# Kernel tuning notes

Hardware: AMD Instinct MI355X
Metric: run time of the kernel (lower is better)

## Reference

```python
import jax, jax.numpy as jnp
import numpy as np

S, B, H = 2048, 16, 512      # seq_len, batch, hidden_size
L = 4096                     # total labels across batch
SMAX = 16                    # max span length
LAB = 256                    # label_size
V = 32000                    # len(voc)


def setup_inputs() -> dict:
    key = jax.random.key(0)
    ks = jax.random.split(key, 10)
    hidden = jax.random.normal(ks[0], (S, B, H), jnp.float32)
    begins = jax.random.randint(ks[1], (L,), 1, S - SMAX - 1)          # >=1 so begin-1 valid
    lens = jax.random.randint(ks[2], (L,), 1, SMAX + 1)                # span length in [1, SMAX]
    ends = begins + lens                                               # < S so hidden[end] valid
    bids = jax.random.randint(ks[3], (L,), 0, B)
    tags = jax.random.randint(ks[4], (L,), 0, V)
    sc = 0.02
    W1 = jax.random.normal(ks[5], (3 * H, LAB), jnp.float32) * sc
    b1 = jnp.zeros((LAB,), jnp.float32)
    W2 = jax.random.normal(ks[6], (LAB, LAB), jnp.float32) * sc
    b2 = jnp.zeros((LAB,), jnp.float32)
    Wo = jax.random.normal(ks[7], (LAB, V), jnp.float32) * sc
    bo = jnp.zeros((V,), jnp.float32)
    return dict(hidden=hidden, begins=begins, ends=ends, bids=bids, tags=tags,
                W1=W1, b1=b1, W2=W2, b2=b2, Wo=Wo, bo=bo)


def reference(hidden, begins, ends, bids, tags, W1, b1, W2, b2, Wo, bo):
    # --- batched span embed: gather + masked mean + boundary concat ---
    pos = begins[:, None] + jnp.arange(SMAX)            # [L, SMAX]
    valid = (pos < ends[:, None]).astype(hidden.dtype)  # [L, SMAX]
    posc = jnp.minimum(pos, S - 1)
    g = hidden[posc, bids[:, None]]                     # [L, SMAX, H] gather
    span_len = (ends - begins).astype(hidden.dtype)[:, None]
    mean = (g * valid[..., None]).sum(axis=1) / span_len           # [L, H]
    left = hidden[begins - 1, bids]                                 # [L, H]
    right = hidden[ends, bids]                                      # [L, H]
    span_emb = jnp.concatenate([left, mean, right], axis=-1)        # [L, 3H]
    # --- hidden2feature: Linear -> sigmoid -> Linear (dropout = eval identity) ---
    feat = jax.nn.sigmoid(span_emb @ W1 + b1) @ W2 + b2             # [L, LAB]
    # --- SoftmaxLoss: -log_softmax(h2o(feat)).gather(tags).mean() per label ---
    logp = jax.nn.log_softmax(feat @ Wo + bo, axis=-1)              # [L, V]
    per_label = -logp[jnp.arange(L), tags]                          # one tag per label
    return per_label.sum() / (L + 1e-5)
```

## Files before the change

### kernel.cpp

```cpp
#include <hip/hip_runtime.h>
#include <math.h>

#define S 2048
#define B 16
#define H 512
#define L 4096
#define SMAX 16
#define LAB 256
#define V 32000
#define NCH 250
#define LOG2E 1.44269504f

typedef __attribute__((ext_vector_type(8))) short short8;
typedef __attribute__((ext_vector_type(4))) float float4v;

__device__ inline ushort f2bf(float x) {
  union { float f; unsigned u; } c; c.f = x;
  unsigned r = c.u + 0x7fffu + ((c.u >> 16) & 1u);
  return (ushort)(r >> 16);
}
__device__ inline float bf2f(ushort h) {
  union { unsigned u; float f; } c; c.u = ((unsigned)h) << 16;
  return c.f;
}

__global__ __launch_bounds__(256) void prep_kernel(
    const float* __restrict__ hidden, const int* __restrict__ begins,
    const int* __restrict__ ends, const int* __restrict__ bids,
    ushort* __restrict__ spanb, const float* __restrict__ W1,
    ushort* __restrict__ W1b, const float* __restrict__ W2,
    ushort* __restrict__ W2b, const float* __restrict__ Wo,
    ushort* __restrict__ Wob) {
  __shared__ ushort tile[64 * 72];
  int bid = blockIdx.x;
  int t = threadIdx.x;

  if (bid < 2048) {
    int sub = t >> 7, tt = t & 127;
    int l = bid * 2 + sub;
    int b = bids[l], s0 = begins[l], s1 = ends[l];
    const float4* hidv = (const float4*)hidden;
    float4 lf = hidv[((size_t)(s0 - 1) * B + b) * 128 + tt];
    float4 rf = hidv[((size_t)s1 * B + b) * 128 + tt];
    float4 m = make_float4(0.f, 0.f, 0.f, 0.f);
    int len = s1 - s0;
    for (int j = 0; j < len; ++j) {
      float4 g = hidv[((size_t)(s0 + j) * B + b) * 128 + tt];
      m.x += g.x; m.y += g.y; m.z += g.z; m.w += g.w;
    }
    float inv = 1.0f / (float)len;
    ushort* sp = spanb + (size_t)l * 1536;
    ushort4 u;
    u.x = f2bf(lf.x); u.y = f2bf(lf.y); u.z = f2bf(lf.z); u.w = f2bf(lf.w);
    *(ushort4*)&sp[tt * 4] = u;
    u.x = f2bf(m.x * inv); u.y = f2bf(m.y * inv);
    u.z = f2bf(m.z * inv); u.w = f2bf(m.w * inv);
    *(ushort4*)&sp[512 + tt * 4] = u;
    u.x = f2bf(rf.x); u.y = f2bf(rf.y); u.z = f2bf(rf.z); u.w = f2bf(rf.w);
    *(ushort4*)&sp[1024 + tt * 4] = u;
    return;
  }

  const float* src; ushort* dst; int K, N, n0, k0; bool wo = false;
  if (bid < 2144) {
    int u = bid - 2048; src = W1; dst = W1b; K = 1536; N = 256;
    n0 = (u & 3) * 64; k0 = (u >> 2) * 64;
  } else if (bid < 2160) {
    int u = bid - 2144; src = W2; dst = W2b; K = 256; N = 256;
    n0 = (u & 3) * 64; k0 = (u >> 2) * 64;
  } else {
    int u = bid - 2160; src = Wo; dst = Wob; K = 256; N = V;
    n0 = (u % 500) * 64; k0 = (u / 500) * 64; wo = true;
  }
  #pragma unroll
  for (int p = 0; p < 16; ++p) {
    int k = p * 4 + (t >> 6);
    int n = t & 63;
    tile[n * 72 + k] = f2bf(src[(size_t)(k0 + k) * N + n0 + n]);
  }
  __syncthreads();
  if (!wo) {
    #pragma unroll
    for (int p = 0; p < 2; ++p) {
      int idx = p * 256 + t;
      int n = idx >> 3, c = idx & 7;
      *(uint4*)&dst[(size_t)(n0 + n) * K + k0 + c * 8] =
          *(const uint4*)&tile[n * 72 + c * 8];
    }
  } else {
    #pragma unroll
    for (int p = 0; p < 2; ++p) {
      int idx = p * 256 + t;
      int n = idx >> 3, c8 = idx & 7;
      int v = n0 + n, k = k0 + c8 * 8;
      int c = v >> 7, nt = (v >> 4) & 7, lr = v & 15;
      int kh = k >> 7, k4 = (k >> 5) & 3, lq = (k >> 3) & 3;
      size_t f = ((((size_t)c * 2 + kh) * 4 + k4) * 8 + nt) * 64 + lq * 16 + lr;
      *(uint4*)&dst[f * 8] = *(const uint4*)&tile[n * 72 + c8 * 8];
    }
  }
}

__global__ __launch_bounds__(256) void feat_mfma_kernel(
    const ushort* __restrict__ spanb, const ushort* __restrict__ W1b,
    const float* __restrict__ b1, const ushort* __restrict__ W2b,
    const float* __restrict__ b2, ushort* __restrict__ featb,
    float* __restrict__ out) {
  __shared__ ushort Hs[16 * 264];
  int tid = threadIdx.x;
  if (blockIdx.x == 0 && tid == 0) *out = 0.f;
  int w = tid >> 6, lane = tid & 63;
  int lr = lane & 15, lq = lane >> 4;
  int l0 = blockIdx.x * 16;

  const short8* arow = (const short8*)(spanb + (size_t)(l0 + lr) * 1536 + lq * 8);
  const short8* brow[4];
  #pragma unroll
  for (int nt = 0; nt < 4; ++nt)
    brow[nt] = (const short8*)(W1b + (size_t)(w * 64 + nt * 16 + lr) * 1536 + lq * 8);

  float4v acc[4];
  float4v zero = {0.f, 0.f, 0.f, 0.f};
  #pragma unroll
  for (int nt = 0; nt < 4; ++nt) acc[nt] = zero;

  short8 af[2], bf[2][4];
  af[0] = arow[0];
  #pragma unroll
  for (int nt = 0; nt < 4; ++nt) bf[0][nt] = brow[nt][0];

  #pragma unroll
  for (int s = 0; s < 48; ++s) {
    int cur = s & 1, nxt = cur ^ 1;
    if (s < 47) {
      af[nxt] = arow[(s + 1) * 4];
      #pragma unroll
      for (int nt = 0; nt < 4; ++nt) bf[nxt][nt] = brow[nt][(s + 1) * 4];
    }
    #pragma unroll
    for (int nt = 0; nt < 4; ++nt)
      acc[nt] = __builtin_amdgcn_mfma_f32_16x16x32_bf16(
          af[cur], bf[cur][nt], acc[nt], 0, 0, 0);
  }

  {
    #pragma unroll
    for (int nt = 0; nt < 4; ++nt) {
      float b1v = b1[w * 64 + nt * 16 + lr];
      #pragma unroll
      for (int r = 0; r < 4; ++r) {
        int row = lq * 4 + r;
        float h = 1.0f / (1.0f + __expf(-(acc[nt][r] + b1v)));
        Hs[row * 264 + w * 64 + nt * 16 + lr] = f2bf(h);
      }
    }
  }
  __syncthreads();

  const short8* wrow[4];
  #pragma unroll
  for (int nt = 0; nt < 4; ++nt)
    wrow[nt] = (const short8*)(W2b + (size_t)(w * 64 + nt * 16 + lr) * 256 + lq * 8);

  float4v acc2[4];
  #pragma unroll
  for (int nt = 0; nt < 4; ++nt) acc2[nt] = zero;

  short8 bf2[2][4];
  #pragma unroll
  for (int nt = 0; nt < 4; ++nt) bf2[0][nt] = wrow[nt][0];

  #pragma unroll
  for (int s = 0; s < 8; ++s) {
    int cur = s & 1, nxt = cur ^ 1;
    if (s < 7) {
      #pragma unroll
      for (int nt = 0; nt < 4; ++nt) bf2[nxt][nt] = wrow[nt][(s + 1) * 4];
    }
    short8 af2 = *(const short8*)&Hs[lr * 264 + s * 32 + lq * 8];
    #pragma unroll
    for (int nt = 0; nt < 4; ++nt)
      acc2[nt] = __builtin_amdgcn_mfma_f32_16x16x32_bf16(
          af2, bf2[cur][nt], acc2[nt], 0, 0, 0);
  }

  {
    #pragma unroll
    for (int nt = 0; nt < 4; ++nt) {
      float b2v = b2[w * 64 + nt * 16 + lr];
      #pragma unroll
      for (int r = 0; r < 4; ++r) {
        int row = lq * 4 + r;
        int col = w * 64 + nt * 16 + lr;
        featb[(size_t)(l0 + row) * 256 + col] = f2bf(acc2[nt][r] + b2v);
      }
    }
  }
}

__global__ __launch_bounds__(512, 4) void logits2_kernel(
    const ushort* __restrict__ featb, const ushort* __restrict__ Wob,
    const float* __restrict__ bo, float* __restrict__ pz) {
  __shared__ ushort Blds[2][16384];
  int tid = threadIdx.x;
  int w = tid >> 6, lane = tid & 63;
  int lr = lane & 15, lq = lane >> 4;
  int l0 = blockIdx.x * 256;
  int v0 = blockIdx.y * 128;

  const short8* aptr[2];
  #pragma unroll
  for (int mt = 0; mt < 2; ++mt)
    aptr[mt] = (const short8*)(featb +
        (size_t)(l0 + w * 32 + mt * 16 + lr) * 256 + lq * 8);

  float4v acc[2][8];
  float4v zero = {0.f, 0.f, 0.f, 0.f};
  #pragma unroll
  for (int mt = 0; mt < 2; ++mt)
    #pragma unroll
    for (int nt = 0; nt < 8; ++nt) acc[mt][nt] = zero;

  short8 af[2][2];
  #pragma unroll
  for (int mt = 0; mt < 2; ++mt) af[0][mt] = aptr[mt][0];

#define STAGE_HALF(buf, kh)                                                   \
  {                                                                           \
    const uint4* src4 = (const uint4*)(Wob +                                  \
        (size_t)blockIdx.y * 32768 + (size_t)(kh) * 16384);                   \
    _Pragma("unroll")                                                         \
    for (int p = 0; p < 4; ++p) {                                             \
      int idx = p * 512 + tid;                                                \
      __builtin_amdgcn_global_load_lds(                                       \
          (const __attribute__((address_space(1))) unsigned int*)(src4 + idx),\
          (__attribute__((address_space(3))) unsigned int*)                   \
              &Blds[buf][(size_t)idx * 8],                                    \
          16, 0, 0);                                                          \
    }                                                                         \
  }

#define KG_BLOCK(buf, kh)                                                     \
  _Pragma("unroll")                                                           \
  for (int k4 = 0; k4 < 4; ++k4) {                                            \
    int kg = (kh) * 4 + k4;                                                   \
    int cur = kg & 1, nxt = cur ^ 1;                                          \
    if (kg < 7) {                                                             \
      _Pragma("unroll")                                                       \
      for (int mt = 0; mt < 2; ++mt)                                          \
        af[nxt][mt] = aptr[mt][(kg + 1) * 4];                                 \
    }                                                                         \
    short8 bf[8];                                                             \
    _Pragma("unroll")                                                         \
    for (int nt = 0; nt < 8; ++nt)                                            \
      bf[nt] = *(const short8*)                                               \
          &Blds[buf][(size_t)(((k4 * 8 + nt) * 64) + lane) * 8];              \
    __builtin_amdgcn_s_setprio(1);                                            \
    _Pragma("unroll")                                                         \
    for (int mt = 0; mt < 2; ++mt)                                            \
      _Pragma("unroll")                                                       \
      for (int nt = 0; nt < 8; ++nt)                                          \
        acc[mt][nt] = __builtin_amdgcn_mfma_f32_16x16x32_bf16(                \
            af[cur][mt], bf[nt], acc[mt][nt], 0, 0, 0);                       \
    __builtin_amdgcn_s_setprio(0);                                            \
  }

  STAGE_HALF(0, 0);
  __syncthreads();
  STAGE_HALF(1, 1);
  KG_BLOCK(0, 0);
  __syncthreads();
  KG_BLOCK(1, 1);

#undef STAGE_HALF
#undef KG_BLOCK

  float bov[8];
  #pragma unroll
  for (int nt = 0; nt < 8; ++nt)
    bov[nt] = bo[v0 + nt * 16 + lr] * LOG2E;
  float z[2][4];
  #pragma unroll
  for (int mt = 0; mt < 2; ++mt)
    #pragma unroll
    for (int r = 0; r < 4; ++r) z[mt][r] = 0.f;
  #pragma unroll
  for (int mt = 0; mt < 2; ++mt)
    #pragma unroll
    for (int nt = 0; nt < 8; ++nt)
      #pragma unroll
      for (int r = 0; r < 4; ++r)
        z[mt][r] += exp2f(fmaf(acc[mt][nt][r], LOG2E, bov[nt]));
  #pragma unroll
  for (int mt = 0; mt < 2; ++mt)
    #pragma unroll
    for (int r = 0; r < 4; ++r) {
      #pragma unroll
      for (int off = 1; off < 16; off <<= 1)
        z[mt][r] += __shfl_xor(z[mt][r], off);
    }
  if (lr == 0) {
    int ch = blockIdx.y;
    #pragma unroll
    for (int mt = 0; mt < 2; ++mt) {
      float4 v4;
      v4.x = z[mt][0]; v4.y = z[mt][1]; v4.z = z[mt][2]; v4.w = z[mt][3];
      *(float4*)&pz[(size_t)ch * L + l0 + w * 32 + mt * 16 + lq * 4] = v4;
    }
  }
}

__global__ __launch_bounds__(256) void tag_kernel(
    const ushort* __restrict__ featb, const ushort* __restrict__ Wob,
    const float* __restrict__ bo, const int* __restrict__ tags,
    float* __restrict__ tagl) {
  int l = blockIdx.x * 4 + (threadIdx.x >> 6);
  int lane = threadIdx.x & 63;
  int tg = tags[l];
  int c = tg >> 7, nt = (tg >> 4) & 7, lr = tg & 15;
  int k0 = lane << 2;
  int kh = k0 >> 7, k4 = (k0 >> 5) & 3, lq = (k0 >> 3) & 3, e = k0 & 7;
  size_t f = ((((size_t)c * 2 + kh) * 4 + k4) * 8 + nt) * 64 + lq * 16 + lr;
  ushort4 wa = *(const ushort4*)&Wob[f * 8 + e];
  ushort4 fa = *(const ushort4*)&featb[(size_t)l * 256 + k0];
  float s = bf2f(fa.x) * bf2f(wa.x) + bf2f(fa.y) * bf2f(wa.y) +
            bf2f(fa.z) * bf2f(wa.z) + bf2f(fa.w) * bf2f(wa.w);
  #pragma unroll
  for (int off = 1; off < 64; off <<= 1) s += __shfl_xor(s, off);
  if (lane == 0) tagl[l] = s + bo[tg];
}

__global__ __launch_bounds__(256) void reduce_kernel(
    const float* __restrict__ pz, const float* __restrict__ tagl,
    float* __restrict__ out) {
  int l = blockIdx.x * 256 + threadIdx.x;
  float z = 0.f;
  #pragma unroll 5
  for (int c = 0; c < NCH; ++c) z += pz[(size_t)c * L + l];
  float per = logf(z) - tagl[l];
  float v = per * (1.0f / (4096.0f + 1e-5f));
  #pragma unroll
  for (int off = 1; off < 64; off <<= 1) v += __shfl_xor(v, off);
  __shared__ float wsum[4];
  if ((threadIdx.x & 63) == 0) wsum[threadIdx.x >> 6] = v;
  __syncthreads();
  if (threadIdx.x == 0)
    atomicAdd(out, wsum[0] + wsum[1] + wsum[2] + wsum[3]);
}

extern "C" void kernel_launch(void* const* d_in, const int* in_sizes, int n_in,
                              void* d_out, int out_size, void* d_ws,
                              size_t ws_size, hipStream_t stream) {
  const float* hidden = (const float*)d_in[0];
  const int* begins = (const int*)d_in[1];
  const int* ends = (const int*)d_in[2];
  const int* bids = (const int*)d_in[3];
  const int* tags = (const int*)d_in[4];
  const float* W1 = (const float*)d_in[5];
  const float* b1 = (const float*)d_in[6];
  const float* W2 = (const float*)d_in[7];
  const float* b2 = (const float*)d_in[8];
  const float* Wo = (const float*)d_in[9];
  const float* bo = (const float*)d_in[10];
  float* out = (float*)d_out;

  ushort* featb = (ushort*)d_ws;
  ushort* Wob = featb + (size_t)L * 256;
  ushort* spanb = Wob + (size_t)V * 256;
  ushort* W1b = spanb + (size_t)L * 1536;
  ushort* W2b = W1b + (size_t)256 * 1536;
  float* pz = (float*)spanb;
  float* tagl = (float*)(W2b + (size_t)256 * 256);

  prep_kernel<<<4160, 256, 0, stream>>>(hidden, begins, ends, bids, spanb,
                                        W1, W1b, W2, W2b, Wo, Wob);
  feat_mfma_kernel<<<256, 256, 0, stream>>>(spanb, W1b, b1, W2b, b2, featb,
                                            out);
  logits2_kernel<<<dim3(16, NCH), 512, 0, stream>>>(featb, Wob, bo, pz);
  tag_kernel<<<L / 4, 256, 0, stream>>>(featb, Wob, bo, tags, tagl);
  reduce_kernel<<<L / 256, 256, 0, stream>>>(pz, tagl, out);
}
```

Baseline: 282.2 us.

## Accumulate softmax partition sums atomically and fuse tag and reduce kernels

The logits kernel now atomically adds each block's partial exp-sum straight into a per-label zsum buffer, which the feature kernel zeroes. This removes the 250-chunk partial array and its separate reduction pass. The tag-logit dot product and the final log/mean reduction are merged into one kernel, saving a launch. The span gather loop is fully unrolled to SMAX with a predicated add, so loads can issue in parallel, at the cost of always reading 16 rows. The atomics add contention and make the summation order nondeterministic.

Measured after the change: 286.9 us. About the same (+1.7%).

```diff
diff --git a/kernel.cpp b/kernel.cpp
--- a/kernel.cpp
+++ b/kernel.cpp
@@ -44,9 +44,10 @@
     float4 rf = hidv[((size_t)s1 * B + b) * 128 + tt];
     float4 m = make_float4(0.f, 0.f, 0.f, 0.f);
     int len = s1 - s0;
-    for (int j = 0; j < len; ++j) {
+    #pragma unroll
+    for (int j = 0; j < SMAX; ++j) {
       float4 g = hidv[((size_t)(s0 + j) * B + b) * 128 + tt];
-      m.x += g.x; m.y += g.y; m.z += g.z; m.w += g.w;
+      if (j < len) { m.x += g.x; m.y += g.y; m.z += g.z; m.w += g.w; }
     }
     float inv = 1.0f / (float)len;
     ushort* sp = spanb + (size_t)l * 1536;
@@ -105,10 +106,11 @@
     const ushort* __restrict__ spanb, const ushort* __restrict__ W1b,
     const float* __restrict__ b1, const ushort* __restrict__ W2b,
     const float* __restrict__ b2, ushort* __restrict__ featb,
-    float* __restrict__ out) {
+    float* __restrict__ zsum, float* __restrict__ out) {
   __shared__ ushort Hs[16 * 264];
   int tid = threadIdx.x;
   if (blockIdx.x == 0 && tid == 0) *out = 0.f;
+  if (tid < 16) zsum[blockIdx.x * 16 + tid] = 0.f;
   int w = tid >> 6, lane = tid & 63;
   int lr = lane & 15, lq = lane >> 4;
   int l0 = blockIdx.x * 16;
@@ -200,7 +202,7 @@
 
 __global__ __launch_bounds__(512, 4) void logits2_kernel(
     const ushort* __restrict__ featb, const ushort* __restrict__ Wob,
-    const float* __restrict__ bo, float* __restrict__ pz) {
+    const float* __restrict__ bo, float* __restrict__ zsum) {
   __shared__ ushort Blds[2][16384];
   int tid = threadIdx.x;
   int w = tid >> 6, lane = tid & 63;
@@ -300,52 +302,46 @@
         z[mt][r] += __shfl_xor(z[mt][r], off);
     }
   if (lr == 0) {
-    int ch = blockIdx.y;
-    #pragma unroll
-    for (int mt = 0; mt < 2; ++mt) {
-      float4 v4;
-      v4.x = z[mt][0]; v4.y = z[mt][1]; v4.z = z[mt][2]; v4.w = z[mt][3];
-      *(float4*)&pz[(size_t)ch * L + l0 + w * 32 + mt * 16 + lq * 4] = v4;
-    }
-  }
-}
-
-__global__ __launch_bounds__(256) void tag_kernel(
+    #pragma unroll
+    for (int mt = 0; mt < 2; ++mt)
+      #pragma unroll
+      for (int r = 0; r < 4; ++r)
+        atomicAdd(&zsum[l0 + w * 32 + mt * 16 + lq * 4 + r], z[mt][r]);
+  }
+}
+
+__global__ __launch_bounds__(256) void final_kernel(
     const ushort* __restrict__ featb, const ushort* __restrict__ Wob,
     const float* __restrict__ bo, const int* __restrict__ tags,
-    float* __restrict__ tagl) {
-  int l = blockIdx.x * 4 + (threadIdx.x >> 6);
-  int lane = threadIdx.x & 63;
-  int tg = tags[l];
-  int c = tg >> 7, nt = (tg >> 4) & 7, lr = tg & 15;
-  int k0 = lane << 2;
-  int kh = k0 >> 7, k4 = (k0 >> 5) & 3, lq = (k0 >> 3) & 3, e = k0 & 7;
-  size_t f = ((((size_t)c * 2 + kh) * 4 + k4) * 8 + nt) * 64 + lq * 16 + lr;
-  ushort4 wa = *(const ushort4*)&Wob[f * 8 + e];
-  ushort4 fa = *(const ushort4*)&featb[(size_t)l * 256 + k0];
-  float s = bf2f(fa.x) * bf2f(wa.x) + bf2f(fa.y) * bf2f(wa.y) +
-            bf2f(fa.z) * bf2f(wa.z) + bf2f(fa.w) * bf2f(wa.w);
-  #pragma unroll
-  for (int off = 1; off < 64; off <<= 1) s += __shfl_xor(s, off);
-  if (lane == 0) tagl[l] = s + bo[tg];
-}
-
-__global__ __launch_bounds__(256) void reduce_kernel(
-    const float* __restrict__ pz, const float* __restrict__ tagl,
-    float* __restrict__ out) {
-  int l = blockIdx.x * 256 + threadIdx.x;
-  float z = 0.f;
-  #pragma unroll 5
-  for (int c = 0; c < NCH; ++c) z += pz[(size_t)c * L + l];
-  float per = logf(z) - tagl[l];
-  float v = per * (1.0f / (4096.0f + 1e-5f));
-  #pragma unroll
-  for (int off = 1; off < 64; off <<= 1) v += __shfl_xor(v, off);
+    const float* __restrict__ zsum, float* __restrict__ out) {
+  int tid = threadIdx.x;
+  int w = tid >> 6, lane = tid & 63;
+  int lb = blockIdx.x * 64;
+  float psum = 0.f;
+  for (int i = 0; i < 16; ++i) {
+    int l = lb + w * 16 + i;
+    int tg = tags[l];
+    int c = tg >> 7, nt = (tg >> 4) & 7, lr = tg & 15;
+    int k0 = lane << 2;
+    int kh = k0 >> 7, k4 = (k0 >> 5) & 3, lq = (k0 >> 3) & 3, e = k0 & 7;
+    size_t f = ((((size_t)c * 2 + kh) * 4 + k4) * 8 + nt) * 64 + lq * 16 + lr;
+    ushort4 wa = *(const ushort4*)&Wob[f * 8 + e];
+    ushort4 fa = *(const ushort4*)&featb[(size_t)l * 256 + k0];
+    float s = bf2f(fa.x) * bf2f(wa.x) + bf2f(fa.y) * bf2f(wa.y) +
+              bf2f(fa.z) * bf2f(wa.z) + bf2f(fa.w) * bf2f(wa.w);
+    #pragma unroll
+    for (int off = 1; off < 64; off <<= 1) s += __shfl_xor(s, off);
+    if (lane == 0)
+      psum += logf(zsum[l]) - (s + bo[tg]);
+  }
   __shared__ float wsum[4];
-  if ((threadIdx.x & 63) == 0) wsum[threadIdx.x >> 6] = v;
-  __syncthreads();
-  if (threadIdx.x == 0)
-    atomicAdd(out, wsum[0] + wsum[1] + wsum[2] + wsum[3]);
+  if (lane == 0) wsum[w] = psum;
+  __syncthreads();
+  if (tid == 0) {
+    float v = (wsum[0] + wsum[1] + wsum[2] + wsum[3]) *
+              (1.0f / (4096.0f + 1e-5f));
+    atomicAdd(out, v);
+  }
 }
 
 extern "C" void kernel_launch(void* const* d_in, const int* in_sizes, int n_in,
@@ -369,14 +365,12 @@
   ushort* spanb = Wob + (size_t)V * 256;
   ushort* W1b = spanb + (size_t)L * 1536;
   ushort* W2b = W1b + (size_t)256 * 1536;
-  float* pz = (float*)spanb;
-  float* tagl = (float*)(W2b + (size_t)256 * 256);
+  float* zsum = (float*)(W2b + (size_t)256 * 256);
 
   prep_kernel<<<4160, 256, 0, stream>>>(hidden, begins, ends, bids, spanb,
                                         W1, W1b, W2, W2b, Wo, Wob);
   feat_mfma_kernel<<<256, 256, 0, stream>>>(spanb, W1b, b1, W2b, b2, featb,
-                                            out);
-  logits2_kernel<<<dim3(16, NCH), 512, 0, stream>>>(featb, Wob, bo, pz);
-  tag_kernel<<<L / 4, 256, 0, stream>>>(featb, Wob, bo, tags, tagl);
-  reduce_kernel<<<L / 256, 256, 0, stream>>>(pz, tagl, out);
-}
+                                            zsum, out);
+  logits2_kernel<<<dim3(16, NCH), 512, 0, stream>>>(featb, Wob, bo, zsum);
+  final_kernel<<<L / 64, 256, 0, stream>>>(featb, Wob, bo, tags, zsum, out);
+}
```
